# Optimization experiments

Measured on AMD Instinct MI355X. Metric: run time of the kernel, lower is better.

Reference implementation:

```python
import jax, jax.numpy as jnp
import numpy as np

V, D, H, DH, FF, L = 512, 256, 8, 32, 2048, 2
B, S = 4, 128
EPS = 1e-5


def setup_inputs() -> dict:
    key = jax.random.key(0)
    ks = jax.random.split(key, 8)
    rn = lambda k, shape: jax.random.normal(k, shape, jnp.float32) * 0.02
    return {
        "x_t": jax.random.randint(ks[0], (B, S), 0, V),
        "emb": rn(ks[1], (V, D)),
        "temperature": jnp.array(1.0, jnp.float32),
        "Wq": rn(ks[2], (L, D, D)), "Wk": rn(ks[3], (L, D, D)),
        "Wv": rn(ks[4], (L, D, D)), "Wo": rn(ks[5], (L, D, D)),
        "bq": jnp.zeros((L, D)), "bk": jnp.zeros((L, D)),
        "bv": jnp.zeros((L, D)), "bo": jnp.zeros((L, D)),
        "W1": rn(ks[6], (L, D, FF)), "b1": jnp.zeros((L, FF)),
        "W2": rn(ks[7], (L, FF, D)), "b2": jnp.zeros((L, D)),
        "ln1_s": jnp.ones((L, D)), "ln1_b": jnp.zeros((L, D)),
        "ln2_s": jnp.ones((L, D)), "ln2_b": jnp.zeros((L, D)),
    }


def _layer_norm(x, scale, bias):
    m = jnp.mean(x, axis=-1, keepdims=True)
    v = jnp.var(x, axis=-1, keepdims=True)
    return (x - m) / jnp.sqrt(v + EPS) * scale + bias


def reference(x_t, emb, temperature, Wq, Wk, Wv, Wo, bq, bk, bv, bo,
              W1, b1, W2, b2, ln1_s, ln1_b, ln2_s, ln2_b):
    b, s = x_t.shape
    x = emb[x_t]  # [B,S,D]
    scale = 1.0 / np.sqrt(DH).astype(np.float32)
    for l in range(L):  # 2 structurally distinct layers (post-norm, ReLU FFN)
        q = (x @ Wq[l] + bq[l]).reshape(b, s, H, DH)
        k = (x @ Wk[l] + bk[l]).reshape(b, s, H, DH)
        v = (x @ Wv[l] + bv[l]).reshape(b, s, H, DH)
        scores = jnp.einsum('bqhd,bkhd->bhqk', q, k) * scale
        attn = jax.nn.softmax(scores, axis=-1)
        o = jnp.einsum('bhqk,bkhd->bqhd', attn, v).reshape(b, s, D)
        x = _layer_norm(x + (o @ Wo[l] + bo[l]), ln1_s[l], ln1_b[l])
        ff = jax.nn.relu(x @ W1[l] + b1[l]) @ W2[l] + b2[l]
        x = _layer_norm(x + ff, ln2_s[l], ln2_b[l])
    sim = (x @ emb.T) / temperature            # [B,S,V]
    tp = jax.nn.softmax(sim, axis=-1)          # [B,S,V]
    # torch loop `trans_matrix[:,:,i,:] = transition_probs` == broadcast over row dim
    return jnp.broadcast_to(tp[:, :, None, :], (b, s, V, V))
```

## Files before the change

### kernel.cpp

```cpp
#include <hip/hip_runtime.h>
#include <math.h>

#define V_  512
#define D_  256
#define H_  8
#define DH_ 32
#define FF_ 2048
#define L_  2
#define B_  4
#define S_  128
#define T_  (B_*S_)

typedef float f32x4 __attribute__((ext_vector_type(4)));
typedef short s16x8 __attribute__((ext_vector_type(8)));
typedef unsigned short u16x4 __attribute__((ext_vector_type(4)));
typedef unsigned short ushort_t;

__device__ __forceinline__ ushort_t f2b(float f) {
    unsigned int u = __builtin_bit_cast(unsigned int, f);
    u += 0x7FFFu + ((u >> 16) & 1u);
    return (ushort_t)(u >> 16);
}
__device__ __forceinline__ float b2f(ushort_t h) {
    unsigned int u = ((unsigned int)h) << 16;
    return __builtin_bit_cast(float, u);
}

__device__ __forceinline__ float waveReduceSum(float v) {
#pragma unroll
    for (int off = 32; off > 0; off >>= 1) v += __shfl_xor(v, off);
    return v;
}
__device__ __forceinline__ float waveReduceMax(float v) {
#pragma unroll
    for (int off = 32; off > 0; off >>= 1) v = fmaxf(v, __shfl_xor(v, off));
    return v;
}

template<int RELU, int OUTB, int BIAS>
__device__ __forceinline__ void mgemm_body(
    const ushort_t* __restrict__ A, const ushort_t* __restrict__ BT,
    const float* __restrict__ bias, float* __restrict__ Cf,
    ushort_t* __restrict__ Cb, int M, int N, int K, int kBegin, int kSteps)
{
    __shared__ ushort_t Al[64][40];
    __shared__ ushort_t Bl[64][40];
    const int tid  = threadIdx.x;
    const int m0   = blockIdx.y * 64, n0 = blockIdx.x * 64;
    const int lane = tid & 63, w = tid >> 6;
    const int srow = tid >> 2, sseg = (tid & 3) * 8;
    const int l15  = lane & 15,  kg = (lane >> 4) * 8;

    f32x4 acc0 = {0.f,0.f,0.f,0.f}, acc1 = acc0, acc2 = acc0, acc3 = acc0;

    for (int kt = 0; kt < kSteps; ++kt) {
        const int k0 = kBegin + kt * 32;
        s16x8 av = *(const s16x8*)&A [(size_t)(m0 + srow) * K + k0 + sseg];
        s16x8 bv = *(const s16x8*)&BT[(size_t)(n0 + srow) * K + k0 + sseg];
        __syncthreads();
        *(s16x8*)&Al[srow][sseg] = av;
        *(s16x8*)&Bl[srow][sseg] = bv;
        __syncthreads();
        s16x8 bfr = *(const s16x8*)&Bl[w * 16 + l15][kg];
        s16x8 a0  = *(const s16x8*)&Al[     l15][kg];
        s16x8 a1  = *(const s16x8*)&Al[16 + l15][kg];
        s16x8 a2  = *(const s16x8*)&Al[32 + l15][kg];
        s16x8 a3  = *(const s16x8*)&Al[48 + l15][kg];
        acc0 = __builtin_amdgcn_mfma_f32_16x16x32_bf16(a0, bfr, acc0, 0, 0, 0);
        acc1 = __builtin_amdgcn_mfma_f32_16x16x32_bf16(a1, bfr, acc1, 0, 0, 0);
        acc2 = __builtin_amdgcn_mfma_f32_16x16x32_bf16(a2, bfr, acc2, 0, 0, 0);
        acc3 = __builtin_amdgcn_mfma_f32_16x16x32_bf16(a3, bfr, acc3, 0, 0, 0);
    }

    const int col = n0 + w * 16 + l15;
    const float bb = BIAS ? bias[col] : 0.f;
    f32x4 accs[4] = {acc0, acc1, acc2, acc3};
#pragma unroll
    for (int r = 0; r < 4; ++r) {
#pragma unroll
        for (int e = 0; e < 4; ++e) {
            const int row = m0 + r * 16 + (lane >> 4) * 4 + e;
            float v = accs[r][e] + bb;
            if (RELU) v = fmaxf(v, 0.f);
            if (OUTB) Cb[(size_t)row * N + col] = f2b(v);
            else      Cf[(size_t)row * N + col] = v;
        }
    }
}

template<int RELU, int OUTB, int BIAS>
__global__ __launch_bounds__(256) void mgemm_k(const ushort_t* A, const ushort_t* BT,
    const float* bias, float* Cf, ushort_t* Cb, int M, int N, int K, int kChunk)
{
    const int z = blockIdx.z;
    mgemm_body<RELU, OUTB, BIAS>(A, BT, bias, Cf + (size_t)z * M * N, Cb,
                                 M, N, K, z * kChunk, kChunk / 32);
}

__global__ __launch_bounds__(256) void qkv_k(const ushort_t* Xb, const ushort_t* WT,
    const float* bq, const float* bk, const float* bv,
    ushort_t* Qb, ushort_t* Kb, ushort_t* Vb)
{
    const int z = blockIdx.z;
    const ushort_t* bt = WT + (size_t)z * (D_ * D_);
    const float* bias; ushort_t* out;
    if (z == 0)      { bias = bq; out = Qb; }
    else if (z == 1) { bias = bk; out = Kb; }
    else             { bias = bv; out = Vb; }
    mgemm_body<0, 1, 1>(Xb, bt, bias, (float*)out, out, T_, D_, D_, 0, D_ / 32);
}

__global__ void embed_k(const int* __restrict__ xt, const float* __restrict__ emb,
                        float* __restrict__ X, ushort_t* __restrict__ Xb,
                        ushort_t* __restrict__ embB)
{
    const int idx = blockIdx.x * 256 + threadIdx.x;
    const int t = idx >> 8, d = idx & 255;
    const float v = emb[(size_t)xt[t] * D_ + d];
    X[idx]  = v;
    Xb[idx] = f2b(v);
    embB[idx] = f2b(emb[idx]);
}

__global__ __launch_bounds__(256) void transw_k(
    const float* __restrict__ Wq, const float* __restrict__ Wk,
    const float* __restrict__ Wv, const float* __restrict__ Wo,
    const float* __restrict__ W1, const float* __restrict__ W2,
    ushort_t* __restrict__ WT, ushort_t* __restrict__ W1T, ushort_t* __restrict__ W2T)
{
    const int id = blockIdx.x;
    const int l  = id >= 1280 ? 1 : 0;
    int t = id - l * 1280;
    const float* src; ushort_t* dst; int R, C, rt, ct;
    if (t < 256) {
        const int kind = t >> 6, tl = t & 63;
        const float* s0 = (kind == 0) ? Wq : (kind == 1) ? Wk : (kind == 2) ? Wv : Wo;
        src = s0 + (size_t)l * (D_ * D_);
        dst = WT + (size_t)l * (4 * D_ * D_) + (size_t)kind * (D_ * D_);
        R = D_; C = D_; rt = tl >> 3; ct = tl & 7;
    } else if (t < 768) {
        const int tl = t - 256;
        src = W1 + (size_t)l * (D_ * FF_); dst = W1T + (size_t)l * (D_ * FF_);
        R = D_; C = FF_; rt = tl >> 6; ct = tl & 63;
    } else {
        const int tl = t - 768;
        src = W2 + (size_t)l * (FF_ * D_); dst = W2T + (size_t)l * (FF_ * D_);
        R = FF_; C = D_; rt = tl >> 3; ct = tl & 7;
    }
    __shared__ float Tl[32][33];
    const int tid = threadIdx.x;
    const int r = tid >> 3, c4 = (tid & 7) * 4;
    f32x4 v = *(const f32x4*)&src[(size_t)(rt * 32 + r) * C + ct * 32 + c4];
    Tl[r][c4] = v[0]; Tl[r][c4 + 1] = v[1]; Tl[r][c4 + 2] = v[2]; Tl[r][c4 + 3] = v[3];
    __syncthreads();
    u16x4 ov;
    ov[0] = f2b(Tl[c4 + 0][r]); ov[1] = f2b(Tl[c4 + 1][r]);
    ov[2] = f2b(Tl[c4 + 2][r]); ov[3] = f2b(Tl[c4 + 3][r]);
    *(u16x4*)&dst[(size_t)(ct * 32 + r) * R + rt * 32 + c4] = ov;
}

__global__ __launch_bounds__(256) void add_ln_k(const float* __restrict__ parts, int nparts,
    const float* __restrict__ bias, float* __restrict__ X, ushort_t* __restrict__ Xb,
    const float* __restrict__ s, const float* __restrict__ b)
{
    __shared__ float red[4];
    const int row = blockIdx.x, tid = threadIdx.x;
    float a = X[(size_t)row * D_ + tid] + bias[tid];
    for (int p = 0; p < nparts; ++p)
        a += parts[(size_t)p * T_ * D_ + (size_t)row * D_ + tid];

    float ws_ = waveReduceSum(a);
    if ((tid & 63) == 0) red[tid >> 6] = ws_;
    __syncthreads();
    const float mean = (red[0] + red[1] + red[2] + red[3]) * (1.f / D_);
    __syncthreads();
    const float d = a - mean;
    float vs = waveReduceSum(d * d);
    if ((tid & 63) == 0) red[tid >> 6] = vs;
    __syncthreads();
    const float var = (red[0] + red[1] + red[2] + red[3]) * (1.f / D_);
    const float y = d * rsqrtf(var + 1e-5f) * s[tid] + b[tid];
    X[(size_t)row * D_ + tid]  = y;
    Xb[(size_t)row * D_ + tid] = f2b(y);
}

__global__ __launch_bounds__(256) void attn_k(const ushort_t* __restrict__ Qb,
    const ushort_t* __restrict__ Kb, const ushort_t* __restrict__ Vb,
    ushort_t* __restrict__ Ob)
{
    __shared__ float Qs[32][36], Ks[128][36], Vs[128][36], Ps[32][132];
    const int bh = blockIdx.x, b = bh >> 3, h = bh & 7;
    const int i0 = blockIdx.y * 32;
    const int tid = threadIdx.x;

#pragma unroll
    for (int it = 0; it < 16; ++it) {
        const int idx = it * 256 + tid, r = idx >> 5, c = idx & 31;
        Ks[r][c] = b2f(Kb[(size_t)(b * S_ + r) * D_ + h * DH_ + c]);
        Vs[r][c] = b2f(Vb[(size_t)(b * S_ + r) * D_ + h * DH_ + c]);
    }
#pragma unroll
    for (int it = 0; it < 4; ++it) {
        const int idx = it * 256 + tid, r = idx >> 5, c = idx & 31;
        Qs[r][c] = b2f(Qb[(size_t)(b * S_ + i0 + r) * D_ + h * DH_ + c]);
    }
    __syncthreads();

    const int i = tid >> 3, jg = tid & 7;
    const float sc = 0.17677669529663687f;
    float sv[16];
    float mx = -1e30f;
#pragma unroll
    for (int jj = 0; jj < 16; ++jj) {
        const int j = jg + jj * 8;
        f32x4 a4 = {0.f,0.f,0.f,0.f};
#pragma unroll
        for (int kk = 0; kk < 8; ++kk) {
            f32x4 q = *(const f32x4*)&Qs[i][kk * 4];
            f32x4 k = *(const f32x4*)&Ks[j][kk * 4];
            a4 += q * k;
        }
        const float sdot = (a4[0] + a4[1] + a4[2] + a4[3]) * sc;
        sv[jj] = sdot;
        mx = fmaxf(mx, sdot);
    }
    mx = fmaxf(mx, __shfl_xor(mx, 1));
    mx = fmaxf(mx, __shfl_xor(mx, 2));
    mx = fmaxf(mx, __shfl_xor(mx, 4));
    float sum = 0.f;
#pragma unroll
    for (int jj = 0; jj < 16; ++jj) {
        const float e = __expf(sv[jj] - mx);
        Ps[i][jg + jj * 8] = e;
        sum += e;
    }
    sum += __shfl_xor(sum, 1);
    sum += __shfl_xor(sum, 2);
    sum += __shfl_xor(sum, 4);
    const float inv = 1.f / sum;
    __syncthreads();

    const int dg = tid & 7;
    f32x4 o = {0.f,0.f,0.f,0.f};
#pragma unroll 4
    for (int j = 0; j < 128; ++j) {
        const float p = Ps[i][j];
        f32x4 vv = *(const f32x4*)&Vs[j][dg * 4];
        o += vv * p;
    }
    u16x4 ov;
    ov[0] = f2b(o[0] * inv); ov[1] = f2b(o[1] * inv);
    ov[2] = f2b(o[2] * inv); ov[3] = f2b(o[3] * inv);
    *(u16x4*)&Ob[(size_t)(b * S_ + i0 + i) * D_ + h * DH_ + dg * 4] = ov;
}

__global__ __launch_bounds__(256) void bcast_k(const float* __restrict__ Lg,
    const float* __restrict__ temp, float* __restrict__ out)
{
    __shared__ float row[V_];
    __shared__ float red[4];
    const int blk = blockIdx.x, t = blk >> 2, quarter = blk & 3;
    const int tid = threadIdx.x;
    const float rT = 1.f / temp[0];
    const float l0 = Lg[(size_t)t * V_ + tid] * rT;
    const float l1 = Lg[(size_t)t * V_ + 256 + tid] * rT;
    float m = waveReduceMax(fmaxf(l0, l1));
    if ((tid & 63) == 0) red[tid >> 6] = m;
    __syncthreads();
    m = fmaxf(fmaxf(red[0], red[1]), fmaxf(red[2], red[3]));
    __syncthreads();
    const float e0 = __expf(l0 - m), e1 = __expf(l1 - m);
    float sblk = waveReduceSum(e0 + e1);
    if ((tid & 63) == 0) red[tid >> 6] = sblk;
    __syncthreads();
    const float inv = 1.f / (red[0] + red[1] + red[2] + red[3]);
    row[tid] = e0 * inv;
    row[tid + 256] = e1 * inv;
    __syncthreads();

    const int c = tid & 127, ihalf = tid >> 7;
    f32x4 v = *(const f32x4*)&row[c * 4];
    f32x4* dst = (f32x4*)out + (size_t)t * V_ * (V_ / 4);
#pragma unroll 4
    for (int r = 0; r < 64; ++r) {
        const int i = quarter * 128 + ihalf + r * 2;
        __builtin_nontemporal_store(v, &dst[(size_t)i * (V_ / 4) + c]);
    }
}

extern "C" void kernel_launch(void* const* d_in, const int* in_sizes, int n_in,
                              void* d_out, int out_size, void* d_ws, size_t ws_size,
                              hipStream_t stream)
{
    const int*   x_t  = (const int*)  d_in[0];
    const float* emb  = (const float*)d_in[1];
    const float* temp = (const float*)d_in[2];
    const float* Wq   = (const float*)d_in[3];
    const float* Wk   = (const float*)d_in[4];
    const float* Wv   = (const float*)d_in[5];
    const float* Wo   = (const float*)d_in[6];
    const float* bq   = (const float*)d_in[7];
    const float* bk   = (const float*)d_in[8];
    const float* bv   = (const float*)d_in[9];
    const float* bo   = (const float*)d_in[10];
    const float* W1   = (const float*)d_in[11];
    const float* b1   = (const float*)d_in[12];
    const float* W2   = (const float*)d_in[13];
    const float* b2   = (const float*)d_in[14];
    const float* ln1s = (const float*)d_in[15];
    const float* ln1b = (const float*)d_in[16];
    const float* ln2s = (const float*)d_in[17];
    const float* ln2b = (const float*)d_in[18];

    float* out = (float*)d_out;
    char*  wsb = (char*)d_ws;

    float*    X    = (float*)   (wsb + 0);
    float*    Part = (float*)   (wsb + 524288);
    float*    Lg   = Part;
    ushort_t* Qb   = (ushort_t*)(wsb + 1572864);
    ushort_t* Kb   = (ushort_t*)(wsb + 1835008);
    ushort_t* Vb   = (ushort_t*)(wsb + 2097152);
    ushort_t* Ob   = (ushort_t*)(wsb + 2359296);
    ushort_t* Xb   = (ushort_t*)(wsb + 2621440);
    ushort_t* Ffb  = (ushort_t*)(wsb + 2883584);
    ushort_t* embB = (ushort_t*)(wsb + 4980736);
    ushort_t* WT   = (ushort_t*)(wsb + 5242880);
    ushort_t* W1T  = (ushort_t*)(wsb + 6291456);
    ushort_t* W2T  = (ushort_t*)(wsb + 8388608);

    embed_k <<<512, 256, 0, stream>>>(x_t, emb, X, Xb, embB);
    transw_k<<<2560, 256, 0, stream>>>(Wq, Wk, Wv, Wo, W1, W2, WT, W1T, W2T);

    for (int l = 0; l < L_; ++l) {
        const ushort_t* WTl  = WT  + (size_t)l * (4 * D_ * D_);
        const ushort_t* W1Tl = W1T + (size_t)l * (D_ * FF_);
        const ushort_t* W2Tl = W2T + (size_t)l * (FF_ * D_);

        qkv_k<<<dim3(4, 8, 3), 256, 0, stream>>>(
            Xb, WTl, bq + l * D_, bk + l * D_, bv + l * D_, Qb, Kb, Vb);

        attn_k<<<dim3(32, 4), 256, 0, stream>>>(Qb, Kb, Vb, Ob);

        mgemm_k<0, 0, 0><<<dim3(4, 8, 1), 256, 0, stream>>>(
            Ob, WTl + 3 * D_ * D_, nullptr, Part, (ushort_t*)Part, T_, D_, D_, D_);
        add_ln_k<<<T_, 256, 0, stream>>>(Part, 1, bo + l * D_, X, Xb,
                                         ln1s + l * D_, ln1b + l * D_);

        mgemm_k<1, 1, 1><<<dim3(32, 8, 1), 256, 0, stream>>>(
            Xb, W1Tl, b1 + l * FF_, Part, Ffb, T_, FF_, D_, D_);

        mgemm_k<0, 0, 0><<<dim3(4, 8, 2), 256, 0, stream>>>(
            Ffb, W2Tl, nullptr, Part, (ushort_t*)Part, T_, D_, FF_, FF_ / 2);
        add_ln_k<<<T_, 256, 0, stream>>>(Part, 2, b2 + l * D_, X, Xb,
                                         ln2s + l * D_, ln2b + l * D_);
    }

    mgemm_k<0, 0, 0><<<dim3(8, 8, 1), 256, 0, stream>>>(
        Xb, embB, nullptr, Lg, (ushort_t*)Lg, T_, V_, D_, D_);

    bcast_k<<<T_ * 4, 256, 0, stream>>>(Lg, temp, out);
}
```

Baseline: 202.6 us.

## Fuse Wo/W2 GEMMs with residual LayerNorm and logits GEMM into broadcast

Merges the embedding and weight-transpose kernels into one launch, and fuses the Wo and W2 projections with bias, residual add and LayerNorm. W2 uses an in-block two-way split-K reduced through shared memory. The logits GEMM is folded into the softmax/broadcast kernel, and attention loads are vectorized. This removes several launches and fp32 partial-buffer round trips, at the cost of only 16 blocks for the fused LN GEMMs and fewer, heavier broadcast blocks.

```diff
diff --git a/kernel.cpp b/kernel.cpp
--- a/kernel.cpp
+++ b/kernel.cpp
@@ -93,8 +93,8 @@
     const float* bias, float* Cf, ushort_t* Cb, int M, int N, int K, int kChunk)
 {
     const int z = blockIdx.z;
-    mgemm_body<RELU, OUTB, BIAS>(A, BT, bias, Cf + (size_t)z * M * N, Cb,
-                                 M, N, K, z * kChunk, kChunk / 32);
+    mgemm_body<RELU, OUTB, BIAS>(A, BT, bias,
+        Cf ? Cf + (size_t)z * M * N : nullptr, Cb, M, N, K, z * kChunk, kChunk / 32);
 }
 
 __global__ __launch_bounds__(256) void qkv_k(const ushort_t* Xb, const ushort_t* WT,
@@ -107,30 +107,31 @@
     if (z == 0)      { bias = bq; out = Qb; }
     else if (z == 1) { bias = bk; out = Kb; }
     else             { bias = bv; out = Vb; }
-    mgemm_body<0, 1, 1>(Xb, bt, bias, (float*)out, out, T_, D_, D_, 0, D_ / 32);
-}
-
-__global__ void embed_k(const int* __restrict__ xt, const float* __restrict__ emb,
-                        float* __restrict__ X, ushort_t* __restrict__ Xb,
-                        ushort_t* __restrict__ embB)
-{
-    const int idx = blockIdx.x * 256 + threadIdx.x;
-    const int t = idx >> 8, d = idx & 255;
-    const float v = emb[(size_t)xt[t] * D_ + d];
-    X[idx]  = v;
-    Xb[idx] = f2b(v);
-    embB[idx] = f2b(emb[idx]);
-}
-
-__global__ __launch_bounds__(256) void transw_k(
+    mgemm_body<0, 1, 1>(Xb, bt, bias, nullptr, out, T_, D_, D_, 0, D_ / 32);
+}
+
+__global__ __launch_bounds__(256) void prep_k(const int* __restrict__ xt,
+    const float* __restrict__ emb, float* __restrict__ X,
+    ushort_t* __restrict__ Xb, ushort_t* __restrict__ embB,
     const float* __restrict__ Wq, const float* __restrict__ Wk,
     const float* __restrict__ Wv, const float* __restrict__ Wo,
     const float* __restrict__ W1, const float* __restrict__ W2,
     ushort_t* __restrict__ WT, ushort_t* __restrict__ W1T, ushort_t* __restrict__ W2T)
 {
-    const int id = blockIdx.x;
+    __shared__ float Tl[32][33];
+    const int tid = threadIdx.x;
+    if (blockIdx.x < 512) {
+        const int idx = blockIdx.x * 256 + tid;
+        const int t = idx >> 8, d = idx & 255;
+        const float v = emb[(size_t)xt[t] * D_ + d];
+        X[idx]  = v;
+        Xb[idx] = f2b(v);
+        embB[idx] = f2b(emb[idx]);
+        return;
+    }
+    const int id = blockIdx.x - 512;
     const int l  = id >= 1280 ? 1 : 0;
-    int t = id - l * 1280;
+    const int t  = id - l * 1280;
     const float* src; ushort_t* dst; int R, C, rt, ct;
     if (t < 256) {
         const int kind = t >> 6, tl = t & 63;
@@ -147,8 +148,6 @@
         src = W2 + (size_t)l * (FF_ * D_); dst = W2T + (size_t)l * (FF_ * D_);
         R = FF_; C = D_; rt = tl >> 3; ct = tl & 7;
     }
-    __shared__ float Tl[32][33];
-    const int tid = threadIdx.x;
     const int r = tid >> 3, c4 = (tid & 7) * 4;
     f32x4 v = *(const f32x4*)&src[(size_t)(rt * 32 + r) * C + ct * 32 + c4];
     Tl[r][c4] = v[0]; Tl[r][c4 + 1] = v[1]; Tl[r][c4 + 2] = v[2]; Tl[r][c4 + 3] = v[3];
@@ -159,31 +158,6 @@
     *(u16x4*)&dst[(size_t)(ct * 32 + r) * R + rt * 32 + c4] = ov;
 }
 
-__global__ __launch_bounds__(256) void add_ln_k(const float* __restrict__ parts, int nparts,
-    const float* __restrict__ bias, float* __restrict__ X, ushort_t* __restrict__ Xb,
-    const float* __restrict__ s, const float* __restrict__ b)
-{
-    __shared__ float red[4];
-    const int row = blockIdx.x, tid = threadIdx.x;
-    float a = X[(size_t)row * D_ + tid] + bias[tid];
-    for (int p = 0; p < nparts; ++p)
-        a += parts[(size_t)p * T_ * D_ + (size_t)row * D_ + tid];
-
-    float ws_ = waveReduceSum(a);
-    if ((tid & 63) == 0) red[tid >> 6] = ws_;
-    __syncthreads();
-    const float mean = (red[0] + red[1] + red[2] + red[3]) * (1.f / D_);
-    __syncthreads();
-    const float d = a - mean;
-    float vs = waveReduceSum(d * d);
-    if ((tid & 63) == 0) red[tid >> 6] = vs;
-    __syncthreads();
-    const float var = (red[0] + red[1] + red[2] + red[3]) * (1.f / D_);
-    const float y = d * rsqrtf(var + 1e-5f) * s[tid] + b[tid];
-    X[(size_t)row * D_ + tid]  = y;
-    Xb[(size_t)row * D_ + tid] = f2b(y);
-}
-
 __global__ __launch_bounds__(256) void attn_k(const ushort_t* __restrict__ Qb,
     const ushort_t* __restrict__ Kb, const ushort_t* __restrict__ Vb,
     ushort_t* __restrict__ Ob)
@@ -194,15 +168,24 @@
     const int tid = threadIdx.x;
 
 #pragma unroll
-    for (int it = 0; it < 16; ++it) {
-        const int idx = it * 256 + tid, r = idx >> 5, c = idx & 31;
-        Ks[r][c] = b2f(Kb[(size_t)(b * S_ + r) * D_ + h * DH_ + c]);
-        Vs[r][c] = b2f(Vb[(size_t)(b * S_ + r) * D_ + h * DH_ + c]);
-    }
-#pragma unroll
-    for (int it = 0; it < 4; ++it) {
-        const int idx = it * 256 + tid, r = idx >> 5, c = idx & 31;
-        Qs[r][c] = b2f(Qb[(size_t)(b * S_ + i0 + r) * D_ + h * DH_ + c]);
+    for (int it = 0; it < 2; ++it) {
+        const int g = it * 256 + tid;
+        const int r = g >> 2, c8 = (g & 3) * 8;
+        s16x8 kv = *(const s16x8*)&Kb[(size_t)(b * S_ + r) * D_ + h * DH_ + c8];
+        s16x8 vv = *(const s16x8*)&Vb[(size_t)(b * S_ + r) * D_ + h * DH_ + c8];
+        f32x4 klo = {b2f((ushort_t)kv[0]), b2f((ushort_t)kv[1]), b2f((ushort_t)kv[2]), b2f((ushort_t)kv[3])};
+        f32x4 khi = {b2f((ushort_t)kv[4]), b2f((ushort_t)kv[5]), b2f((ushort_t)kv[6]), b2f((ushort_t)kv[7])};
+        f32x4 vlo = {b2f((ushort_t)vv[0]), b2f((ushort_t)vv[1]), b2f((ushort_t)vv[2]), b2f((ushort_t)vv[3])};
+        f32x4 vhi = {b2f((ushort_t)vv[4]), b2f((ushort_t)vv[5]), b2f((ushort_t)vv[6]), b2f((ushort_t)vv[7])};
+        *(f32x4*)&Ks[r][c8]     = klo;  *(f32x4*)&Ks[r][c8 + 4] = khi;
+        *(f32x4*)&Vs[r][c8]     = vlo;  *(f32x4*)&Vs[r][c8 + 4] = vhi;
+    }
+    if (tid < 128) {
+        const int r = tid >> 2, c8 = (tid & 3) * 8;
+        s16x8 qv = *(const s16x8*)&Qb[(size_t)(b * S_ + i0 + r) * D_ + h * DH_ + c8];
+        f32x4 qlo = {b2f((ushort_t)qv[0]), b2f((ushort_t)qv[1]), b2f((ushort_t)qv[2]), b2f((ushort_t)qv[3])};
+        f32x4 qhi = {b2f((ushort_t)qv[4]), b2f((ushort_t)qv[5]), b2f((ushort_t)qv[6]), b2f((ushort_t)qv[7])};
+        *(f32x4*)&Qs[r][c8] = qlo;  *(f32x4*)&Qs[r][c8 + 4] = qhi;
     }
     __syncthreads();
 
@@ -254,37 +237,246 @@
     *(u16x4*)&Ob[(size_t)(b * S_ + i0 + i) * D_ + h * DH_ + dg * 4] = ov;
 }
 
-__global__ __launch_bounds__(256) void bcast_k(const float* __restrict__ Lg,
-    const float* __restrict__ temp, float* __restrict__ out)
-{
+__global__ __launch_bounds__(256) void woln_k(
+    const ushort_t* __restrict__ A, const ushort_t* __restrict__ BT,
+    const float* __restrict__ bias, float* __restrict__ X,
+    ushort_t* __restrict__ Xb, const float* __restrict__ lns,
+    const float* __restrict__ lnb)
+{
+    __shared__ ushort_t As[32][40];
+    __shared__ ushort_t Bs[256][40];
+    __shared__ float Ct[32][272];
+    const int tid = threadIdx.x;
+    const int m0 = blockIdx.x * 32;
+    const int w = tid >> 6, lane = tid & 63;
+    const int l15 = lane & 15, kgrp = (lane >> 4) * 8;
+
+    f32x4 acc[2][4] = {};
+    const int ar = tid >> 2, aseg = tid & 3;
+
+    for (int t = 0; t < 8; ++t) {
+        const int k0 = t * 32;
+        s16x8 av;
+        if (tid < 128) av = *(const s16x8*)&A[(size_t)(m0 + ar) * D_ + k0 + aseg * 8];
+        s16x8 bv[4];
+#pragma unroll
+        for (int i = 0; i < 4; ++i) {
+            const int c = tid + i * 256;
+            bv[i] = *(const s16x8*)&BT[(size_t)(c >> 2) * D_ + k0 + (c & 3) * 8];
+        }
+        __syncthreads();
+        if (tid < 128) *(s16x8*)&As[ar][aseg * 8] = av;
+#pragma unroll
+        for (int i = 0; i < 4; ++i) {
+            const int c = tid + i * 256;
+            *(s16x8*)&Bs[c >> 2][(c & 3) * 8] = bv[i];
+        }
+        __syncthreads();
+        s16x8 bf[4], af[2];
+#pragma unroll
+        for (int j = 0; j < 4; ++j) bf[j] = *(const s16x8*)&Bs[w * 64 + j * 16 + l15][kgrp];
+#pragma unroll
+        for (int r = 0; r < 2; ++r) af[r] = *(const s16x8*)&As[r * 16 + l15][kgrp];
+#pragma unroll
+        for (int r = 0; r < 2; ++r)
+#pragma unroll
+            for (int j = 0; j < 4; ++j)
+                acc[r][j] = __builtin_amdgcn_mfma_f32_16x16x32_bf16(af[r], bf[j], acc[r][j], 0, 0, 0);
+    }
+    __syncthreads();
+#pragma unroll
+    for (int r = 0; r < 2; ++r)
+#pragma unroll
+        for (int j = 0; j < 4; ++j)
+#pragma unroll
+            for (int e = 0; e < 4; ++e)
+                Ct[r * 16 + (lane >> 4) * 4 + e][w * 64 + j * 16 + l15] = acc[r][j][e];
+    __syncthreads();
+
+    const int row = tid >> 3, c0 = (tid & 7) * 32;
+    const int grow = m0 + row;
+    float a[32];
+    float sum = 0.f;
+#pragma unroll
+    for (int c = 0; c < 32; ++c) {
+        a[c] = Ct[row][c0 + c] + X[(size_t)grow * D_ + c0 + c] + bias[c0 + c];
+        sum += a[c];
+    }
+    sum += __shfl_xor(sum, 1); sum += __shfl_xor(sum, 2); sum += __shfl_xor(sum, 4);
+    const float mean = sum * (1.f / D_);
+    float vs = 0.f;
+#pragma unroll
+    for (int c = 0; c < 32; ++c) { const float d = a[c] - mean; vs += d * d; }
+    vs += __shfl_xor(vs, 1); vs += __shfl_xor(vs, 2); vs += __shfl_xor(vs, 4);
+    const float rstd = rsqrtf(vs * (1.f / D_) + 1e-5f);
+#pragma unroll
+    for (int c4 = 0; c4 < 8; ++c4) {
+        f32x4 y4; u16x4 yb;
+#pragma unroll
+        for (int e = 0; e < 4; ++e) {
+            const int c = c4 * 4 + e;
+            const float y = (a[c] - mean) * rstd * lns[c0 + c] + lnb[c0 + c];
+            y4[e] = y; yb[e] = f2b(y);
+        }
+        *(f32x4*)&X [(size_t)grow * D_ + c0 + c4 * 4] = y4;
+        *(u16x4*)&Xb[(size_t)grow * D_ + c0 + c4 * 4] = yb;
+    }
+}
+
+__global__ __launch_bounds__(512) void w2ln_k(
+    const ushort_t* __restrict__ A, const ushort_t* __restrict__ BT,
+    const float* __restrict__ bias, float* __restrict__ X,
+    ushort_t* __restrict__ Xb, const float* __restrict__ lns,
+    const float* __restrict__ lnb)
+{
+    __shared__ __align__(16) char ubuf[46080];
+    ushort_t (*As)[40] = (ushort_t (*)[40])ubuf;
+    ushort_t (*Bs)[40] = (ushort_t (*)[40])(ubuf + 5120);
+    float    (*Ct)[272] = (float (*)[272])ubuf;
+
+    const int tid = threadIdx.x;
+    const int m0 = blockIdx.x * 32;
+    const int w = tid >> 6, lane = tid & 63;
+    const int kg = w >> 2, ng = w & 3;
+    const int l15 = lane & 15, kgrp = (lane >> 4) * 8;
+
+    f32x4 acc[2][4] = {};
+    const int akg = tid >> 7, arr = (tid >> 2) & 31, aseg = tid & 3;
+
+    for (int t = 0; t < 32; ++t) {
+        s16x8 av, bv[4];
+        if (tid < 256)
+            av = *(const s16x8*)&A[(size_t)(m0 + arr) * FF_ + akg * 1024 + t * 32 + aseg * 8];
+#pragma unroll
+        for (int i = 0; i < 4; ++i) {
+            const int c = tid + i * 512;
+            const int bkg = c >> 10, br = (c >> 2) & 255, bseg = c & 3;
+            bv[i] = *(const s16x8*)&BT[(size_t)br * FF_ + bkg * 1024 + t * 32 + bseg * 8];
+        }
+        __syncthreads();
+        if (tid < 256) *(s16x8*)&As[akg * 32 + arr][aseg * 8] = av;
+#pragma unroll
+        for (int i = 0; i < 4; ++i) {
+            const int c = tid + i * 512;
+            const int bkg = c >> 10, br = (c >> 2) & 255, bseg = c & 3;
+            *(s16x8*)&Bs[bkg * 256 + br][bseg * 8] = bv[i];
+        }
+        __syncthreads();
+        s16x8 bf[4], af[2];
+#pragma unroll
+        for (int j = 0; j < 4; ++j) bf[j] = *(const s16x8*)&Bs[kg * 256 + ng * 64 + j * 16 + l15][kgrp];
+#pragma unroll
+        for (int r = 0; r < 2; ++r) af[r] = *(const s16x8*)&As[kg * 32 + r * 16 + l15][kgrp];
+#pragma unroll
+        for (int r = 0; r < 2; ++r)
+#pragma unroll
+            for (int j = 0; j < 4; ++j)
+                acc[r][j] = __builtin_amdgcn_mfma_f32_16x16x32_bf16(af[r], bf[j], acc[r][j], 0, 0, 0);
+    }
+    __syncthreads();
+    if (kg == 0) {
+#pragma unroll
+        for (int r = 0; r < 2; ++r)
+#pragma unroll
+            for (int j = 0; j < 4; ++j)
+#pragma unroll
+                for (int e = 0; e < 4; ++e)
+                    Ct[r * 16 + (lane >> 4) * 4 + e][ng * 64 + j * 16 + l15] = acc[r][j][e];
+    }
+    __syncthreads();
+    if (kg == 1) {
+#pragma unroll
+        for (int r = 0; r < 2; ++r)
+#pragma unroll
+            for (int j = 0; j < 4; ++j)
+#pragma unroll
+                for (int e = 0; e < 4; ++e)
+                    Ct[r * 16 + (lane >> 4) * 4 + e][ng * 64 + j * 16 + l15] += acc[r][j][e];
+    }
+    __syncthreads();
+
+    const int row = tid >> 4, c0 = (tid & 15) * 16;
+    const int grow = m0 + row;
+    float a[16];
+    float sum = 0.f;
+#pragma unroll
+    for (int c = 0; c < 16; ++c) {
+        a[c] = Ct[row][c0 + c] + X[(size_t)grow * D_ + c0 + c] + bias[c0 + c];
+        sum += a[c];
+    }
+    sum += __shfl_xor(sum, 1); sum += __shfl_xor(sum, 2);
+    sum += __shfl_xor(sum, 4); sum += __shfl_xor(sum, 8);
+    const float mean = sum * (1.f / D_);
+    float vs = 0.f;
+#pragma unroll
+    for (int c = 0; c < 16; ++c) { const float d = a[c] - mean; vs += d * d; }
+    vs += __shfl_xor(vs, 1); vs += __shfl_xor(vs, 2);
+    vs += __shfl_xor(vs, 4); vs += __shfl_xor(vs, 8);
+    const float rstd = rsqrtf(vs * (1.f / D_) + 1e-5f);
+#pragma unroll
+    for (int c4 = 0; c4 < 4; ++c4) {
+        f32x4 y4; u16x4 yb;
+#pragma unroll
+        for (int e = 0; e < 4; ++e) {
+            const int c = c4 * 4 + e;
+            const float y = (a[c] - mean) * rstd * lns[c0 + c] + lnb[c0 + c];
+            y4[e] = y; yb[e] = f2b(y);
+        }
+        *(f32x4*)&X [(size_t)grow * D_ + c0 + c4 * 4] = y4;
+        *(u16x4*)&Xb[(size_t)grow * D_ + c0 + c4 * 4] = yb;
+    }
+}
+
+__global__ __launch_bounds__(256) void bcast_k(const ushort_t* __restrict__ Xb,
+    const ushort_t* __restrict__ embB, const float* __restrict__ temp,
+    float* __restrict__ out)
+{
+    __shared__ float xrow[D_];
     __shared__ float row[V_];
     __shared__ float red[4];
-    const int blk = blockIdx.x, t = blk >> 2, quarter = blk & 3;
-    const int tid = threadIdx.x;
+    const int t = blockIdx.x, tid = threadIdx.x;
+    xrow[tid] = b2f(Xb[(size_t)t * D_ + tid]);
+    __syncthreads();
+
     const float rT = 1.f / temp[0];
-    const float l0 = Lg[(size_t)t * V_ + tid] * rT;
-    const float l1 = Lg[(size_t)t * V_ + 256 + tid] * rT;
+    float l0 = 0.f, l1 = 0.f;
+    {
+        const ushort_t* e0p = &embB[(size_t)tid * D_];
+        const ushort_t* e1p = &embB[(size_t)(tid + 256) * D_];
+#pragma unroll 8
+        for (int cc = 0; cc < 32; ++cc) {
+            s16x8 a0 = *(const s16x8*)&e0p[cc * 8];
+            s16x8 a1 = *(const s16x8*)&e1p[cc * 8];
+#pragma unroll
+            for (int e = 0; e < 8; ++e) {
+                const float xe = xrow[cc * 8 + e];
+                l0 = fmaf(xe, b2f((ushort_t)a0[e]), l0);
+                l1 = fmaf(xe, b2f((ushort_t)a1[e]), l1);
+            }
+        }
+        l0 *= rT; l1 *= rT;
+    }
     float m = waveReduceMax(fmaxf(l0, l1));
     if ((tid & 63) == 0) red[tid >> 6] = m;
     __syncthreads();
     m = fmaxf(fmaxf(red[0], red[1]), fmaxf(red[2], red[3]));
     __syncthreads();
     const float e0 = __expf(l0 - m), e1 = __expf(l1 - m);
-    float sblk = waveReduceSum(e0 + e1);
-    if ((tid & 63) == 0) red[tid >> 6] = sblk;
+    float s = waveReduceSum(e0 + e1);
+    if ((tid & 63) == 0) red[tid >> 6] = s;
     __syncthreads();
     const float inv = 1.f / (red[0] + red[1] + red[2] + red[3]);
-    row[tid] = e0 * inv;
+    row[tid]       = e0 * inv;
     row[tid + 256] = e1 * inv;
     __syncthreads();
 
-    const int c = tid & 127, ihalf = tid >> 7;
-    f32x4 v = *(const f32x4*)&row[c * 4];
+    const int c = tid & 127, rh = tid >> 7;
+    f32x4 v4 = *(const f32x4*)&row[c * 4];
     f32x4* dst = (f32x4*)out + (size_t)t * V_ * (V_ / 4);
 #pragma unroll 4
-    for (int r = 0; r < 64; ++r) {
-        const int i = quarter * 128 + ihalf + r * 2;
-        __builtin_nontemporal_store(v, &dst[(size_t)i * (V_ / 4) + c]);
+    for (int it = 0; it < 256; ++it) {
+        const int i = it * 2 + rh;
+        __builtin_nontemporal_store(v4, &dst[(size_t)i * (V_ / 4) + c]);
     }
 }
 
@@ -316,21 +508,19 @@
     char*  wsb = (char*)d_ws;
 
     float*    X    = (float*)   (wsb + 0);
-    float*    Part = (float*)   (wsb + 524288);
-    float*    Lg   = Part;
-    ushort_t* Qb   = (ushort_t*)(wsb + 1572864);
-    ushort_t* Kb   = (ushort_t*)(wsb + 1835008);
-    ushort_t* Vb   = (ushort_t*)(wsb + 2097152);
-    ushort_t* Ob   = (ushort_t*)(wsb + 2359296);
-    ushort_t* Xb   = (ushort_t*)(wsb + 2621440);
-    ushort_t* Ffb  = (ushort_t*)(wsb + 2883584);
-    ushort_t* embB = (ushort_t*)(wsb + 4980736);
-    ushort_t* WT   = (ushort_t*)(wsb + 5242880);
-    ushort_t* W1T  = (ushort_t*)(wsb + 6291456);
-    ushort_t* W2T  = (ushort_t*)(wsb + 8388608);
-
-    embed_k <<<512, 256, 0, stream>>>(x_t, emb, X, Xb, embB);
-    transw_k<<<2560, 256, 0, stream>>>(Wq, Wk, Wv, Wo, W1, W2, WT, W1T, W2T);
+    ushort_t* Qb   = (ushort_t*)(wsb + 524288);
+    ushort_t* Kb   = (ushort_t*)(wsb + 786432);
+    ushort_t* Vb   = (ushort_t*)(wsb + 1048576);
+    ushort_t* Ob   = (ushort_t*)(wsb + 1310720);
+    ushort_t* Xb   = (ushort_t*)(wsb + 1572864);
+    ushort_t* Ffb  = (ushort_t*)(wsb + 1835008);
+    ushort_t* embB = (ushort_t*)(wsb + 3932160);
+    ushort_t* WT   = (ushort_t*)(wsb + 4194304);
+    ushort_t* W1T  = (ushort_t*)(wsb + 5242880);
+    ushort_t* W2T  = (ushort_t*)(wsb + 7340032);
+
+    prep_k<<<3072, 256, 0, stream>>>(x_t, emb, X, Xb, embB,
+                                     Wq, Wk, Wv, Wo, W1, W2, WT, W1T, W2T);
 
     for (int l = 0; l < L_; ++l) {
         const ushort_t* WTl  = WT  + (size_t)l * (4 * D_ * D_);
@@ -342,22 +532,15 @@
 
         attn_k<<<dim3(32, 4), 256, 0, stream>>>(Qb, Kb, Vb, Ob);
 
-        mgemm_k<0, 0, 0><<<dim3(4, 8, 1), 256, 0, stream>>>(
-            Ob, WTl + 3 * D_ * D_, nullptr, Part, (ushort_t*)Part, T_, D_, D_, D_);
-        add_ln_k<<<T_, 256, 0, stream>>>(Part, 1, bo + l * D_, X, Xb,
-                                         ln1s + l * D_, ln1b + l * D_);
+        woln_k<<<16, 256, 0, stream>>>(Ob, WTl + 3 * D_ * D_, bo + l * D_,
+                                       X, Xb, ln1s + l * D_, ln1b + l * D_);
 
         mgemm_k<1, 1, 1><<<dim3(32, 8, 1), 256, 0, stream>>>(
-            Xb, W1Tl, b1 + l * FF_, Part, Ffb, T_, FF_, D_, D_);
-
-        mgemm_k<0, 0, 0><<<dim3(4, 8, 2), 256, 0, stream>>>(
-            Ffb, W2Tl, nullptr, Part, (ushort_t*)Part, T_, D_, FF_, FF_ / 2);
-        add_ln_k<<<T_, 256, 0, stream>>>(Part, 2, b2 + l * D_, X, Xb,
-                                         ln2s + l * D_, ln2b + l * D_);
-    }
-
-    mgemm_k<0, 0, 0><<<dim3(8, 8, 1), 256, 0, stream>>>(
-        Xb, embB, nullptr, Lg, (ushort_t*)Lg, T_, V_, D_, D_);
-
-    bcast_k<<<T_ * 4, 256, 0, stream>>>(Lg, temp, out);
-}
+            Xb, W1Tl, b1 + l * FF_, nullptr, Ffb, T_, FF_, D_, D_);
+
+        w2ln_k<<<16, 512, 0, stream>>>(Ffb, W2Tl, b2 + l * D_,
+                                       X, Xb, ln2s + l * D_, ln2b + l * D_);
+    }
+
+    bcast_k<<<512, 256, 0, stream>>>(Xb, embB, temp, out);
+}
```

Result: slower. 250.2 us (+23.5%).

## Merge prep kernels, split W2 GEMM 4-way, vectorize attention loads

Applied to the files above, without the earlier changes.

Fuses the embedding and weight-transpose kernels into one prep launch to drop a launch. Raises the split-K factor of the FFN down-projection from 2 to 4, writing partials into two workspace regions that reuse the Q buffer area, so more blocks can run in parallel. The add+layernorm kernel now sums those partials. The attention kernel loads Q/K/V with 16-byte vector loads instead of scalar bf16 loads. The cost is extra partial-sum traffic and reuse of the Q/K region for partials.

```diff
diff --git a/kernel.cpp b/kernel.cpp
--- a/kernel.cpp
+++ b/kernel.cpp
@@ -90,11 +90,15 @@
 
 template<int RELU, int OUTB, int BIAS>
 __global__ __launch_bounds__(256) void mgemm_k(const ushort_t* A, const ushort_t* BT,
-    const float* bias, float* Cf, ushort_t* Cb, int M, int N, int K, int kChunk)
+    const float* bias, float* Cf0, float* Cf1, ushort_t* Cb,
+    int M, int N, int K, int kChunk)
 {
     const int z = blockIdx.z;
-    mgemm_body<RELU, OUTB, BIAS>(A, BT, bias, Cf + (size_t)z * M * N, Cb,
-                                 M, N, K, z * kChunk, kChunk / 32);
+    float* Cfz = nullptr;
+    if (Cf0) Cfz = (z < 2) ? Cf0 + (size_t)z * M * N
+                           : Cf1 + (size_t)(z - 2) * M * N;
+    mgemm_body<RELU, OUTB, BIAS>(A, BT, bias, Cfz, Cb, M, N, K,
+                                 z * kChunk, kChunk / 32);
 }
 
 __global__ __launch_bounds__(256) void qkv_k(const ushort_t* Xb, const ushort_t* WT,
@@ -107,30 +111,31 @@
     if (z == 0)      { bias = bq; out = Qb; }
     else if (z == 1) { bias = bk; out = Kb; }
     else             { bias = bv; out = Vb; }
-    mgemm_body<0, 1, 1>(Xb, bt, bias, (float*)out, out, T_, D_, D_, 0, D_ / 32);
-}
-
-__global__ void embed_k(const int* __restrict__ xt, const float* __restrict__ emb,
-                        float* __restrict__ X, ushort_t* __restrict__ Xb,
-                        ushort_t* __restrict__ embB)
-{
-    const int idx = blockIdx.x * 256 + threadIdx.x;
-    const int t = idx >> 8, d = idx & 255;
-    const float v = emb[(size_t)xt[t] * D_ + d];
-    X[idx]  = v;
-    Xb[idx] = f2b(v);
-    embB[idx] = f2b(emb[idx]);
-}
-
-__global__ __launch_bounds__(256) void transw_k(
+    mgemm_body<0, 1, 1>(Xb, bt, bias, nullptr, out, T_, D_, D_, 0, D_ / 32);
+}
+
+__global__ __launch_bounds__(256) void prep_k(const int* __restrict__ xt,
+    const float* __restrict__ emb, float* __restrict__ X,
+    ushort_t* __restrict__ Xb, ushort_t* __restrict__ embB,
     const float* __restrict__ Wq, const float* __restrict__ Wk,
     const float* __restrict__ Wv, const float* __restrict__ Wo,
     const float* __restrict__ W1, const float* __restrict__ W2,
     ushort_t* __restrict__ WT, ushort_t* __restrict__ W1T, ushort_t* __restrict__ W2T)
 {
-    const int id = blockIdx.x;
+    __shared__ float Tl[32][33];
+    const int tid = threadIdx.x;
+    if (blockIdx.x < 512) {
+        const int idx = blockIdx.x * 256 + tid;
+        const int t = idx >> 8, d = idx & 255;
+        const float v = emb[(size_t)xt[t] * D_ + d];
+        X[idx]  = v;
+        Xb[idx] = f2b(v);
+        embB[idx] = f2b(emb[idx]);
+        return;
+    }
+    const int id = blockIdx.x - 512;
     const int l  = id >= 1280 ? 1 : 0;
-    int t = id - l * 1280;
+    const int t  = id - l * 1280;
     const float* src; ushort_t* dst; int R, C, rt, ct;
     if (t < 256) {
         const int kind = t >> 6, tl = t & 63;
@@ -147,8 +152,6 @@
         src = W2 + (size_t)l * (FF_ * D_); dst = W2T + (size_t)l * (FF_ * D_);
         R = FF_; C = D_; rt = tl >> 3; ct = tl & 7;
     }
-    __shared__ float Tl[32][33];
-    const int tid = threadIdx.x;
     const int r = tid >> 3, c4 = (tid & 7) * 4;
     f32x4 v = *(const f32x4*)&src[(size_t)(rt * 32 + r) * C + ct * 32 + c4];
     Tl[r][c4] = v[0]; Tl[r][c4 + 1] = v[1]; Tl[r][c4 + 2] = v[2]; Tl[r][c4 + 3] = v[3];
@@ -159,15 +162,18 @@
     *(u16x4*)&dst[(size_t)(ct * 32 + r) * R + rt * 32 + c4] = ov;
 }
 
-__global__ __launch_bounds__(256) void add_ln_k(const float* __restrict__ parts, int nparts,
-    const float* __restrict__ bias, float* __restrict__ X, ushort_t* __restrict__ Xb,
-    const float* __restrict__ s, const float* __restrict__ b)
+__global__ __launch_bounds__(256) void add_ln_k(
+    const float* __restrict__ p0, const float* __restrict__ p1, int nparts,
+    const float* __restrict__ bias, float* __restrict__ X,
+    ushort_t* __restrict__ Xb, const float* __restrict__ s,
+    const float* __restrict__ b)
 {
     __shared__ float red[4];
     const int row = blockIdx.x, tid = threadIdx.x;
-    float a = X[(size_t)row * D_ + tid] + bias[tid];
-    for (int p = 0; p < nparts; ++p)
-        a += parts[(size_t)p * T_ * D_ + (size_t)row * D_ + tid];
+    const size_t off = (size_t)row * D_ + tid;
+    const size_t TD = (size_t)T_ * D_;
+    float a = X[off] + bias[tid] + p0[off];
+    if (nparts == 4) a += p0[TD + off] + p1[off] + p1[TD + off];
 
     float ws_ = waveReduceSum(a);
     if ((tid & 63) == 0) red[tid >> 6] = ws_;
@@ -180,8 +186,8 @@
     __syncthreads();
     const float var = (red[0] + red[1] + red[2] + red[3]) * (1.f / D_);
     const float y = d * rsqrtf(var + 1e-5f) * s[tid] + b[tid];
-    X[(size_t)row * D_ + tid]  = y;
-    Xb[(size_t)row * D_ + tid] = f2b(y);
+    X[off]  = y;
+    Xb[off] = f2b(y);
 }
 
 __global__ __launch_bounds__(256) void attn_k(const ushort_t* __restrict__ Qb,
@@ -194,15 +200,24 @@
     const int tid = threadIdx.x;
 
 #pragma unroll
-    for (int it = 0; it < 16; ++it) {
-        const int idx = it * 256 + tid, r = idx >> 5, c = idx & 31;
-        Ks[r][c] = b2f(Kb[(size_t)(b * S_ + r) * D_ + h * DH_ + c]);
-        Vs[r][c] = b2f(Vb[(size_t)(b * S_ + r) * D_ + h * DH_ + c]);
-    }
-#pragma unroll
-    for (int it = 0; it < 4; ++it) {
-        const int idx = it * 256 + tid, r = idx >> 5, c = idx & 31;
-        Qs[r][c] = b2f(Qb[(size_t)(b * S_ + i0 + r) * D_ + h * DH_ + c]);
+    for (int it = 0; it < 2; ++it) {
+        const int g = it * 256 + tid;
+        const int r = g >> 2, c8 = (g & 3) * 8;
+        s16x8 kv = *(const s16x8*)&Kb[(size_t)(b * S_ + r) * D_ + h * DH_ + c8];
+        s16x8 vv = *(const s16x8*)&Vb[(size_t)(b * S_ + r) * D_ + h * DH_ + c8];
+        f32x4 klo = {b2f((ushort_t)kv[0]), b2f((ushort_t)kv[1]), b2f((ushort_t)kv[2]), b2f((ushort_t)kv[3])};
+        f32x4 khi = {b2f((ushort_t)kv[4]), b2f((ushort_t)kv[5]), b2f((ushort_t)kv[6]), b2f((ushort_t)kv[7])};
+        f32x4 vlo = {b2f((ushort_t)vv[0]), b2f((ushort_t)vv[1]), b2f((ushort_t)vv[2]), b2f((ushort_t)vv[3])};
+        f32x4 vhi = {b2f((ushort_t)vv[4]), b2f((ushort_t)vv[5]), b2f((ushort_t)vv[6]), b2f((ushort_t)vv[7])};
+        *(f32x4*)&Ks[r][c8]     = klo;  *(f32x4*)&Ks[r][c8 + 4] = khi;
+        *(f32x4*)&Vs[r][c8]     = vlo;  *(f32x4*)&Vs[r][c8 + 4] = vhi;
+    }
+    if (tid < 128) {
+        const int r = tid >> 2, c8 = (tid & 3) * 8;
+        s16x8 qv = *(const s16x8*)&Qb[(size_t)(b * S_ + i0 + r) * D_ + h * DH_ + c8];
+        f32x4 qlo = {b2f((ushort_t)qv[0]), b2f((ushort_t)qv[1]), b2f((ushort_t)qv[2]), b2f((ushort_t)qv[3])};
+        f32x4 qhi = {b2f((ushort_t)qv[4]), b2f((ushort_t)qv[5]), b2f((ushort_t)qv[6]), b2f((ushort_t)qv[7])};
+        *(f32x4*)&Qs[r][c8] = qlo;  *(f32x4*)&Qs[r][c8 + 4] = qhi;
     }
     __syncthreads();
 
@@ -315,22 +330,23 @@
     float* out = (float*)d_out;
     char*  wsb = (char*)d_ws;
 
-    float*    X    = (float*)   (wsb + 0);
-    float*    Part = (float*)   (wsb + 524288);
-    float*    Lg   = Part;
-    ushort_t* Qb   = (ushort_t*)(wsb + 1572864);
-    ushort_t* Kb   = (ushort_t*)(wsb + 1835008);
-    ushort_t* Vb   = (ushort_t*)(wsb + 2097152);
-    ushort_t* Ob   = (ushort_t*)(wsb + 2359296);
-    ushort_t* Xb   = (ushort_t*)(wsb + 2621440);
-    ushort_t* Ffb  = (ushort_t*)(wsb + 2883584);
-    ushort_t* embB = (ushort_t*)(wsb + 4980736);
-    ushort_t* WT   = (ushort_t*)(wsb + 5242880);
-    ushort_t* W1T  = (ushort_t*)(wsb + 6291456);
-    ushort_t* W2T  = (ushort_t*)(wsb + 8388608);
-
-    embed_k <<<512, 256, 0, stream>>>(x_t, emb, X, Xb, embB);
-    transw_k<<<2560, 256, 0, stream>>>(Wq, Wk, Wv, Wo, W1, W2, WT, W1T, W2T);
+    float*    X     = (float*)   (wsb + 0);
+    float*    PartA = (float*)   (wsb + 524288);
+    float*    Lg    = PartA;
+    ushort_t* Qb    = (ushort_t*)(wsb + 1572864);
+    float*    PartB = (float*)   (wsb + 1572864);
+    ushort_t* Kb    = (ushort_t*)(wsb + 1835008);
+    ushort_t* Vb    = (ushort_t*)(wsb + 2097152);
+    ushort_t* Ob    = (ushort_t*)(wsb + 2359296);
+    ushort_t* Xb    = (ushort_t*)(wsb + 2621440);
+    ushort_t* Ffb   = (ushort_t*)(wsb + 2883584);
+    ushort_t* embB  = (ushort_t*)(wsb + 4980736);
+    ushort_t* WT    = (ushort_t*)(wsb + 5242880);
+    ushort_t* W1T   = (ushort_t*)(wsb + 6291456);
+    ushort_t* W2T   = (ushort_t*)(wsb + 8388608);
+
+    prep_k<<<3072, 256, 0, stream>>>(x_t, emb, X, Xb, embB,
+                                     Wq, Wk, Wv, Wo, W1, W2, WT, W1T, W2T);
 
     for (int l = 0; l < L_; ++l) {
         const ushort_t* WTl  = WT  + (size_t)l * (4 * D_ * D_);
@@ -343,21 +359,22 @@
         attn_k<<<dim3(32, 4), 256, 0, stream>>>(Qb, Kb, Vb, Ob);
 
         mgemm_k<0, 0, 0><<<dim3(4, 8, 1), 256, 0, stream>>>(
-            Ob, WTl + 3 * D_ * D_, nullptr, Part, (ushort_t*)Part, T_, D_, D_, D_);
-        add_ln_k<<<T_, 256, 0, stream>>>(Part, 1, bo + l * D_, X, Xb,
-                                         ln1s + l * D_, ln1b + l * D_);
+            Ob, WTl + 3 * D_ * D_, nullptr, PartA, nullptr, nullptr,
+            T_, D_, D_, D_);
+        add_ln_k<<<T_, 256, 0, stream>>>(PartA, nullptr, 1, bo + l * D_,
+                                         X, Xb, ln1s + l * D_, ln1b + l * D_);
 
         mgemm_k<1, 1, 1><<<dim3(32, 8, 1), 256, 0, stream>>>(
-            Xb, W1Tl, b1 + l * FF_, Part, Ffb, T_, FF_, D_, D_);
-
-        mgemm_k<0, 0, 0><<<dim3(4, 8, 2), 256, 0, stream>>>(
-            Ffb, W2Tl, nullptr, Part, (ushort_t*)Part, T_, D_, FF_, FF_ / 2);
-        add_ln_k<<<T_, 256, 0, stream>>>(Part, 2, b2 + l * D_, X, Xb,
-                                         ln2s + l * D_, ln2b + l * D_);
+            Xb, W1Tl, b1 + l * FF_, nullptr, nullptr, Ffb, T_, FF_, D_, D_);
+
+        mgemm_k<0, 0, 0><<<dim3(4, 8, 4), 256, 0, stream>>>(
+            Ffb, W2Tl, nullptr, PartA, PartB, nullptr, T_, D_, FF_, FF_ / 4);
+        add_ln_k<<<T_, 256, 0, stream>>>(PartA, PartB, 4, b2 + l * D_,
+                                         X, Xb, ln2s + l * D_, ln2b + l * D_);
     }
 
     mgemm_k<0, 0, 0><<<dim3(8, 8, 1), 256, 0, stream>>>(
-        Xb, embB, nullptr, Lg, (ushort_t*)Lg, T_, V_, D_, D_);
+        Xb, embB, nullptr, Lg, nullptr, nullptr, T_, V_, D_, D_);
 
     bcast_k<<<T_ * 4, 256, 0, stream>>>(Lg, temp, out);
 }
```

After: 187.9 us. 7.3% less time.
